# Optimization experiments

Measured on AMD Instinct MI355X. Metric: run time of the kernel, lower is better.

The kernel has to match this reference:

```python
import jax, jax.numpy as jnp
import numpy as np

VOCAB, EMB, UNITS = 50000, 512, 1024
B, T = 2048, 80

def setup_inputs() -> dict:
    key = jax.random.key(0)
    ks = jax.random.split(key, 10)
    s_e = 1.0 / np.sqrt(EMB)
    s_u = 1.0 / np.sqrt(UNITS)
    return {
        "tokens": jax.random.randint(ks[0], (B, T), 0, VOCAB),
        "emb": jax.random.normal(ks[1], (VOCAB, EMB), jnp.float32) * 0.05,
        "W1": jax.random.normal(ks[2], (EMB, UNITS), jnp.float32) * s_e,
        "U1": jax.random.normal(ks[3], (UNITS, UNITS), jnp.float32) * s_u,
        "b1": jnp.zeros((UNITS,), jnp.float32),
        "W2": jax.random.normal(ks[4], (UNITS, UNITS), jnp.float32) * s_u,
        "U2": jax.random.normal(ks[5], (UNITS, UNITS), jnp.float32) * s_u,
        "b2": jnp.zeros((UNITS,), jnp.float32),
        "Wo": jax.random.normal(ks[6], (UNITS, 1), jnp.float32) * s_u,
        "bo": jnp.zeros((1,), jnp.float32),
    }

def _simple_rnn(x_tbd, W, U, b):
    # x_tbd: [T, B, D] time-major input; SimpleRNN: h_t = tanh(x_t W + h_{t-1} U + b)
    B_ = x_tbd.shape[1]
    h0 = jnp.zeros((B_, U.shape[0]), x_tbd.dtype)
    xw = jnp.einsum('tbd,du->tbu', x_tbd, W) + b  # precompute input projection
    def step(h, xw_t):
        h = jnp.tanh(xw_t + h @ U)
        return h, h
    h_last, hs = jax.lax.scan(step, h0, xw)
    return h_last, hs  # hs: [T, B, U]

def reference(tokens, emb, W1, U1, b1, W2, U2, b2, Wo, bo):
    x = emb[tokens]                       # [B, T, E]
    x = jnp.transpose(x, (1, 0, 2))       # [T, B, E] time-major
    _, hs1 = _simple_rnn(x, W1, U1, b1)   # [T, B, U] (return_sequences=True)
    h2, _ = _simple_rnn(hs1, W2, U2, b2)  # [B, U] last state
    logits = h2 @ Wo + bo                 # [B, 1]
    return jax.nn.sigmoid(logits)
```

## Files before the change

kernel.cpp:

```cpp
#include <hip/hip_runtime.h>
#include <math.h>

#define M_TOTAL 2048
#define N_TOTAL 1024
#define TSEQ    80
#define EMB_D   512
#define VOCAB   50000
#define BK      64

typedef __attribute__((ext_vector_type(8))) short bf16x8;
typedef __attribute__((ext_vector_type(4))) float f32x4;

__device__ __forceinline__ ushort f2bf(float f) {
    union { float f; unsigned u; } v; v.f = f;
    unsigned r = v.u + 0x7FFFu + ((v.u >> 16) & 1u);
    return (ushort)(r >> 16);
}
__device__ __forceinline__ float bf2f(ushort h) {
    union { unsigned u; float f; } v; v.u = ((unsigned)h) << 16;
    return v.f;
}
__device__ __forceinline__ void gload_lds16(const ushort* g, ushort* l) {
    __builtin_amdgcn_global_load_lds(
        (const __attribute__((address_space(1))) void*)g,
        (__attribute__((address_space(3))) void*)l, 16, 0, 0);
}
#define VMC6()  asm volatile("s_waitcnt vmcnt(6)" ::: "memory")
#define VMC0()  asm volatile("s_waitcnt vmcnt(0)" ::: "memory")
#define SBAR()  __builtin_amdgcn_s_barrier()
#define SCHED0() __builtin_amdgcn_sched_barrier(0)

__global__ __launch_bounds__(256) void fused_step(
    ushort* __restrict__ xw_h1,
    const ushort* __restrict__ h1prev,
    const ushort* __restrict__ U1T, const float* __restrict__ b1,
    ushort* __restrict__ h2n, const ushort* __restrict__ h2c,
    const ushort* __restrict__ W2T, const ushort* __restrict__ U2T,
    const float* __restrict__ b2, int do_l1, int do_l2)
{
    __shared__ ushort As[3][128 * BK];
    __shared__ ushort Bs[3][64 * BK];
    const int tid = threadIdx.x;
    const int w = tid >> 6, l = tid & 63;
    const int wr = w >> 1, wc = w & 1;
    const int bid = blockIdx.x;
    const int strip = bid & 7;
    const int q = bid >> 3;
    const int layer = q & 1;
    const int rr = q >> 1;
    const int n = strip * 2 + (rr & 1);
    const int m = rr >> 1;
    const int bm0 = m << 7;
    const int bn0 = n << 6;

    if (layer ? !do_l2 : !do_l1) return;

    const int lr = l >> 3;
    const int se = ((l & 7) ^ lr) << 3;

    auto stage = [&](const ushort* __restrict__ A, const ushort* __restrict__ B,
                     int k0, int buf) {
        #pragma unroll
        for (int j = 0; j < 4; ++j) {
            const int rb = w * 32 + j * 8;
            gload_lds16(A + (size_t)(bm0 + rb + lr) * N_TOTAL + k0 + se,
                        &As[buf][rb * BK + l * 8]);
        }
        #pragma unroll
        for (int j = 0; j < 2; ++j) {
            const int rb = w * 16 + j * 8;
            gload_lds16(B + (size_t)(bn0 + rb + lr) * N_TOTAL + k0 + se,
                        &Bs[buf][rb * BK + l * 8]);
        }
    };

    f32x4 acc[4][2] = {};

    auto compute = [&](int buf) {
        #pragma unroll
        for (int kf = 0; kf < 2; ++kf) {
            const int ke = kf * 32 + (l >> 4) * 8;
            bf16x8 a[4], b[2];
            #pragma unroll
            for (int mf = 0; mf < 4; ++mf) {
                const int row = wr * 64 + mf * 16 + (l & 15);
                a[mf] = *(const bf16x8*)&As[buf][row * BK + (ke ^ ((row & 7) << 3))];
            }
            #pragma unroll
            for (int nf = 0; nf < 2; ++nf) {
                const int row = wc * 32 + nf * 16 + (l & 15);
                b[nf] = *(const bf16x8*)&Bs[buf][row * BK + (ke ^ ((row & 7) << 3))];
            }
            #pragma unroll
            for (int mf = 0; mf < 4; ++mf)
                #pragma unroll
                for (int nf = 0; nf < 2; ++nf)
                    acc[mf][nf] = __builtin_amdgcn_mfma_f32_16x16x32_bf16(
                        a[mf], b[nf], acc[mf][nf], 0, 0, 0);
        }
    };

    if (layer == 0) {
        auto stage_cc = [&](int cc, int buf) { stage(h1prev, U1T, cc << 6, buf); };
        stage_cc(0, 0);
        int bufc = 0;
        #pragma unroll
        for (int c = 0; c < 16; ++c) {
            int bufn = bufc + 1; if (bufn == 3) bufn = 0;
            if (c + 1 < 16) { stage_cc(c + 1, bufn); VMC6(); }
            else            { VMC0(); }
            SBAR(); SCHED0();
            compute(bufc);
            bufc = bufn;
        }
        #pragma unroll
        for (int nf = 0; nf < 2; ++nf) {
            const int col = bn0 + wc * 32 + nf * 16 + (l & 15);
            const float bz = b1[col];
            #pragma unroll
            for (int mf = 0; mf < 4; ++mf) {
                const int rb = bm0 + wr * 64 + mf * 16 + (l >> 4) * 4;
                #pragma unroll
                for (int r = 0; r < 4; ++r) {
                    const size_t idx = (size_t)(rb + r) * N_TOTAL + col;
                    xw_h1[idx] = f2bf(tanhf(acc[mf][nf][r] + bf2f(xw_h1[idx]) + bz));
                }
            }
        }
    } else {
        auto stage_cc = [&](int cc, int buf) {
            if (cc < 16) stage(h1prev, W2T, cc << 6, buf);
            else         stage(h2c,    U2T, (cc - 16) << 6, buf);
        };
        stage_cc(0, 0);
        int bufc = 0;
        #pragma unroll
        for (int c = 0; c < 32; ++c) {
            int bufn = bufc + 1; if (bufn == 3) bufn = 0;
            if (c + 1 < 32) { stage_cc(c + 1, bufn); VMC6(); }
            else            { VMC0(); }
            SBAR(); SCHED0();
            compute(bufc);
            bufc = bufn;
        }
        #pragma unroll
        for (int nf = 0; nf < 2; ++nf) {
            const int col = bn0 + wc * 32 + nf * 16 + (l & 15);
            const float bz = b2[col];
            #pragma unroll
            for (int mf = 0; mf < 4; ++mf) {
                const int rb = bm0 + wr * 64 + mf * 16 + (l >> 4) * 4;
                #pragma unroll
                for (int r = 0; r < 4; ++r)
                    h2n[(size_t)(rb + r) * N_TOTAL + col] =
                        f2bf(tanhf(acc[mf][nf][r] + bz));
            }
        }
    }
}

__global__ __launch_bounds__(256) void xw1_gemm(
    ushort* __restrict__ outp,
    const ushort* __restrict__ embb,
    const int* __restrict__ tok,
    const ushort* __restrict__ W1T)
{
    __shared__ ushort As[3][128 * BK];
    __shared__ ushort Bs[3][64 * BK];
    const int tid = threadIdx.x;
    const int w = tid >> 6, l = tid & 63;
    const int wr = w >> 1, wc = w & 1;
    const int bid = blockIdx.x;
    const int strip = bid & 7;
    const int q = bid >> 3;
    const int n = strip * 2 + (q & 1);
    const int m = q >> 1;
    const int bm0 = m << 7;
    const int bn0 = n << 6;

    const int lr = l >> 3;
    const int se = ((l & 7) ^ lr) << 3;

    size_t ga[4];
    #pragma unroll
    for (int j = 0; j < 4; ++j) {
        const int rg = bm0 + w * 32 + j * 8 + lr;
        const int token = tok[(rg & (M_TOTAL - 1)) * TSEQ + (rg >> 11)];
        ga[j] = (size_t)token * EMB_D + se;
    }

    auto stage = [&](int cc, int buf) {
        const int k0 = cc << 6;
        #pragma unroll
        for (int j = 0; j < 4; ++j)
            gload_lds16(embb + ga[j] + k0, &As[buf][(w * 32 + j * 8) * BK + l * 8]);
        #pragma unroll
        for (int j = 0; j < 2; ++j) {
            const int rb = w * 16 + j * 8;
            gload_lds16(W1T + (size_t)(bn0 + rb + lr) * EMB_D + k0 + se,
                        &Bs[buf][rb * BK + l * 8]);
        }
    };

    f32x4 acc[4][2] = {};
    stage(0, 0);
    int bufc = 0;
    #pragma unroll
    for (int c = 0; c < 8; ++c) {
        int bufn = bufc + 1; if (bufn == 3) bufn = 0;
        if (c + 1 < 8) { stage(c + 1, bufn); VMC6(); }
        else           { VMC0(); }
        SBAR(); SCHED0();
        #pragma unroll
        for (int kf = 0; kf < 2; ++kf) {
            const int ke = kf * 32 + (l >> 4) * 8;
            bf16x8 a[4], b[2];
            #pragma unroll
            for (int mf = 0; mf < 4; ++mf) {
                const int row = wr * 64 + mf * 16 + (l & 15);
                a[mf] = *(const bf16x8*)&As[bufc][row * BK + (ke ^ ((row & 7) << 3))];
            }
            #pragma unroll
            for (int nf = 0; nf < 2; ++nf) {
                const int row = wc * 32 + nf * 16 + (l & 15);
                b[nf] = *(const bf16x8*)&Bs[bufc][row * BK + (ke ^ ((row & 7) << 3))];
            }
            #pragma unroll
            for (int mf = 0; mf < 4; ++mf)
                #pragma unroll
                for (int nf = 0; nf < 2; ++nf)
                    acc[mf][nf] = __builtin_amdgcn_mfma_f32_16x16x32_bf16(
                        a[mf], b[nf], acc[mf][nf], 0, 0, 0);
        }
        bufc = bufn;
    }

    #pragma unroll
    for (int nf = 0; nf < 2; ++nf) {
        const int col = bn0 + wc * 32 + nf * 16 + (l & 15);
        #pragma unroll
        for (int mf = 0; mf < 4; ++mf) {
            const int rb = bm0 + wr * 64 + mf * 16 + (l >> 4) * 4;
            #pragma unroll
            for (int r = 0; r < 4; ++r)
                outp[(size_t)(rb + r) * N_TOTAL + col] = f2bf(acc[mf][nf][r]);
        }
    }
}

__global__ __launch_bounds__(256) void emb_convert(
    ushort* __restrict__ dst, const float* __restrict__ src)
{
    const size_t i = ((size_t)blockIdx.x * 256 + threadIdx.x) * 8;
    const float4 v0 = *(const float4*)(src + i);
    const float4 v1 = *(const float4*)(src + i + 4);
    const unsigned w0 = f2bf(v0.x) | (f2bf(v0.y) << 16);
    const unsigned w1 = f2bf(v0.z) | (f2bf(v0.w) << 16);
    const unsigned w2 = f2bf(v1.x) | (f2bf(v1.y) << 16);
    const unsigned w3 = f2bf(v1.z) | (f2bf(v1.w) << 16);
    *(uint4*)(dst + i) = make_uint4(w0, w1, w2, w3);
}

__global__ __launch_bounds__(256) void transpose_convert(
    ushort* __restrict__ outT, const float* __restrict__ in, int K, int N)
{
    __shared__ float tile[64][65];
    const int tiles_n = N >> 6;
    const int k0 = (blockIdx.x / tiles_n) << 6;
    const int n0 = (blockIdx.x % tiles_n) << 6;
    const int tid = threadIdx.x;
    const int r = tid >> 4, c = (tid & 15) << 2;
    #pragma unroll
    for (int i = 0; i < 4; ++i) {
        const float4 v = *(const float4*)(in + (size_t)(k0 + r + i * 16) * N + n0 + c);
        tile[r + i * 16][c + 0] = v.x;
        tile[r + i * 16][c + 1] = v.y;
        tile[r + i * 16][c + 2] = v.z;
        tile[r + i * 16][c + 3] = v.w;
    }
    __syncthreads();
    const int n = tid >> 2, ks = (tid & 3) << 4;
    unsigned pk[8];
    #pragma unroll
    for (int j = 0; j < 8; ++j) {
        const unsigned lo = f2bf(tile[ks + 2 * j][n]);
        const unsigned hi = f2bf(tile[ks + 2 * j + 1][n]);
        pk[j] = lo | (hi << 16);
    }
    ushort* dst = outT + (size_t)(n0 + n) * K + k0 + ks;
    *(uint4*)(dst + 0) = make_uint4(pk[0], pk[1], pk[2], pk[3]);
    *(uint4*)(dst + 8) = make_uint4(pk[4], pk[5], pk[6], pk[7]);
}

__global__ __launch_bounds__(256) void out_kernel(
    float* __restrict__ out, const ushort* __restrict__ h2,
    const float* __restrict__ Wo, const float* __restrict__ bo)
{
    const int row  = blockIdx.x * 4 + (threadIdx.x >> 6);
    const int lane = threadIdx.x & 63;
    const ushort* hr = h2 + (size_t)row * N_TOTAL;
    float s = 0.f;
    for (int k = lane; k < N_TOTAL; k += 64)
        s += bf2f(hr[k]) * Wo[k];
    #pragma unroll
    for (int off = 32; off; off >>= 1)
        s += __shfl_down(s, off);
    if (lane == 0)
        out[row] = 1.f / (1.f + expf(-(s + bo[0])));
}

extern "C" void kernel_launch(void* const* d_in, const int* in_sizes, int n_in,
                              void* d_out, int out_size, void* d_ws, size_t ws_size,
                              hipStream_t stream) {
    const int*   tokens = (const int*)  d_in[0];
    const float* emb    = (const float*)d_in[1];
    const float* W1     = (const float*)d_in[2];
    const float* U1     = (const float*)d_in[3];
    const float* b1     = (const float*)d_in[4];
    const float* W2     = (const float*)d_in[5];
    const float* U2     = (const float*)d_in[6];
    const float* b2     = (const float*)d_in[7];
    const float* Wo     = (const float*)d_in[8];
    const float* bo     = (const float*)d_in[9];
    float* out = (float*)d_out;

    char* ws = (char*)d_ws;
    const size_t HB   = (size_t)M_TOTAL * N_TOTAL * sizeof(ushort);
    const size_t SLAB = (size_t)M_TOTAL * N_TOTAL;
    ushort* h1zero = (ushort*)(ws);
    ushort* h2a    = (ushort*)(ws + 1 * HB);
    ushort* h2b    = (ushort*)(ws + 2 * HB);
    size_t off = 3 * HB;
    ushort* W1T = (ushort*)(ws + off); off += (size_t)N_TOTAL * EMB_D   * 2;
    ushort* U1T = (ushort*)(ws + off); off += (size_t)N_TOTAL * N_TOTAL * 2;
    ushort* W2T = (ushort*)(ws + off); off += (size_t)N_TOTAL * N_TOTAL * 2;
    ushort* U2T = (ushort*)(ws + off); off += (size_t)N_TOTAL * N_TOTAL * 2;
    ushort* embb = (ushort*)(ws + off); off += (size_t)VOCAB * EMB_D * 2;
    ushort* XW1  = (ushort*)(ws + off);

    hipMemsetAsync(h1zero, 0, HB, stream);
    hipMemsetAsync(h2a,    0, HB, stream);

    emb_convert<<<dim3(12500), 256, 0, stream>>>(embb, emb);
    transpose_convert<<<dim3((EMB_D  / 64) * (N_TOTAL / 64)), 256, 0, stream>>>(W1T, W1, EMB_D,   N_TOTAL);
    transpose_convert<<<dim3((N_TOTAL / 64) * (N_TOTAL / 64)), 256, 0, stream>>>(U1T, U1, N_TOTAL, N_TOTAL);
    transpose_convert<<<dim3((N_TOTAL / 64) * (N_TOTAL / 64)), 256, 0, stream>>>(W2T, W2, N_TOTAL, N_TOTAL);
    transpose_convert<<<dim3((N_TOTAL / 64) * (N_TOTAL / 64)), 256, 0, stream>>>(U2T, U2, N_TOTAL, N_TOTAL);

    xw1_gemm<<<dim3((TSEQ * M_TOTAL / 128) * 16), 256, 0, stream>>>(XW1, embb, tokens, W1T);

    ushort* h2c = h2a; ushort* h2n = h2b;
    for (int i = 0; i <= TSEQ; ++i) {
        const int do_l1 = (i < TSEQ) ? 1 : 0;
        const int do_l2 = (i >= 1) ? 1 : 0;
        ushort* slab_i  = (i < TSEQ) ? (XW1 + (size_t)i * SLAB) : XW1;
        const ushort* h1prev = (i == 0) ? h1zero : (XW1 + (size_t)(i - 1) * SLAB);
        fused_step<<<dim3(512), 256, 0, stream>>>(
            slab_i, h1prev, U1T, b1, h2n, h2c, W2T, U2T, b2, do_l1, do_l2);
        if (i >= 1) { ushort* t = h2c; h2c = h2n; h2n = t; }
    }

    out_kernel<<<dim3(M_TOTAL / 4), dim3(256), 0, stream>>>(out, h2c, Wo, bo);
}
```

Measured before the change: 2.428 ms.

## Precompute embedding-projection table, gather per step, and pipeline layer-2 projection separately

Replaces the per-token input projection GEMM (T*B rows) with a GEMM over the vocabulary (emb@W1, about 50k rows) followed by per-step row gathers into a three-slot ring buffer. The layer-2 input projection h1@W2 is split from the recurrent h2@U2 GEMM and skewed across steps with an fp32 intermediate. This lets three independent 128x128-tile GEMM jobs plus a gather run in one launch per step. Tiles grow to 128x128 with a new double/triple-buffered staging schedule. The cost is extra fp32 traffic for the xw2 buffers and a large EW1 table, in exchange for removing the large XW1 GEMM and halving the serial K-depth of the layer-2 work per step.

```diff
diff --git a/kernel.cpp b/kernel.cpp
--- a/kernel.cpp
+++ b/kernel.cpp
@@ -6,6 +6,7 @@
 #define TSEQ    80
 #define EMB_D   512
 #define VOCAB   50000
+#define EW_ROWS 50048
 #define BK      64
 
 typedef __attribute__((ext_vector_type(8))) short bf16x8;
@@ -25,227 +26,196 @@
         (const __attribute__((address_space(1))) void*)g,
         (__attribute__((address_space(3))) void*)l, 16, 0, 0);
 }
-#define VMC6()  asm volatile("s_waitcnt vmcnt(6)" ::: "memory")
+#define VMC4()  asm volatile("s_waitcnt vmcnt(4)" ::: "memory")
 #define VMC0()  asm volatile("s_waitcnt vmcnt(0)" ::: "memory")
 #define SBAR()  __builtin_amdgcn_s_barrier()
 #define SCHED0() __builtin_amdgcn_sched_barrier(0)
 
-__global__ __launch_bounds__(256) void fused_step(
-    ushort* __restrict__ xw_h1,
-    const ushort* __restrict__ h1prev,
-    const ushort* __restrict__ U1T, const float* __restrict__ b1,
-    ushort* __restrict__ h2n, const ushort* __restrict__ h2c,
-    const ushort* __restrict__ W2T, const ushort* __restrict__ U2T,
-    const float* __restrict__ b2, int do_l1, int do_l2)
-{
-    __shared__ ushort As[3][128 * BK];
-    __shared__ ushort Bs[3][64 * BK];
-    const int tid = threadIdx.x;
-    const int w = tid >> 6, l = tid & 63;
+template<int NC>
+__device__ __forceinline__ void gemm_core(
+    f32x4 (&acc)[4][4],
+    const ushort* __restrict__ A, const size_t* __restrict__ ga,
+    const ushort* __restrict__ B, const size_t* __restrict__ gb,
+    int w, int l,
+    ushort (*As)[128 * BK], ushort (*Bs)[128 * BK])
+{
     const int wr = w >> 1, wc = w & 1;
-    const int bid = blockIdx.x;
-    const int strip = bid & 7;
-    const int q = bid >> 3;
-    const int layer = q & 1;
-    const int rr = q >> 1;
-    const int n = strip * 2 + (rr & 1);
-    const int m = rr >> 1;
-    const int bm0 = m << 7;
-    const int bn0 = n << 6;
-
-    if (layer ? !do_l2 : !do_l1) return;
-
-    const int lr = l >> 3;
-    const int se = ((l & 7) ^ lr) << 3;
-
-    auto stage = [&](const ushort* __restrict__ A, const ushort* __restrict__ B,
-                     int k0, int buf) {
-        #pragma unroll
-        for (int j = 0; j < 4; ++j) {
-            const int rb = w * 32 + j * 8;
-            gload_lds16(A + (size_t)(bm0 + rb + lr) * N_TOTAL + k0 + se,
-                        &As[buf][rb * BK + l * 8]);
-        }
-        #pragma unroll
-        for (int j = 0; j < 2; ++j) {
-            const int rb = w * 16 + j * 8;
-            gload_lds16(B + (size_t)(bn0 + rb + lr) * N_TOTAL + k0 + se,
-                        &Bs[buf][rb * BK + l * 8]);
-        }
+    auto stA = [&](int c, int buf) {
+        const int k0 = c << 6;
+        #pragma unroll
+        for (int j = 0; j < 4; ++j)
+            gload_lds16(A + ga[j] + k0, &As[buf][(w * 32 + j * 8) * BK + l * 8]);
     };
-
-    f32x4 acc[4][2] = {};
-
-    auto compute = [&](int buf) {
+    auto stB = [&](int c, int buf) {
+        const int k0 = c << 6;
+        #pragma unroll
+        for (int j = 0; j < 4; ++j)
+            gload_lds16(B + gb[j] + k0, &Bs[buf][(w * 32 + j * 8) * BK + l * 8]);
+    };
+    stA(0, 0); stB(0, 0); stA(1, 1);
+    #pragma unroll
+    for (int c = 0; c < NC; ++c) {
+        if (c + 1 < NC) { VMC4(); } else { VMC0(); }
+        SBAR(); SCHED0();
+        if (c + 1 < NC) stB(c + 1, (c + 1) & 1);
+        if (c + 2 < NC) stA(c + 2, (c + 2) % 3);
         #pragma unroll
         for (int kf = 0; kf < 2; ++kf) {
             const int ke = kf * 32 + (l >> 4) * 8;
-            bf16x8 a[4], b[2];
+            bf16x8 a[4], b[4];
             #pragma unroll
             for (int mf = 0; mf < 4; ++mf) {
                 const int row = wr * 64 + mf * 16 + (l & 15);
-                a[mf] = *(const bf16x8*)&As[buf][row * BK + (ke ^ ((row & 7) << 3))];
+                a[mf] = *(const bf16x8*)&As[c % 3][row * BK + (ke ^ ((row & 7) << 3))];
             }
             #pragma unroll
-            for (int nf = 0; nf < 2; ++nf) {
-                const int row = wc * 32 + nf * 16 + (l & 15);
-                b[nf] = *(const bf16x8*)&Bs[buf][row * BK + (ke ^ ((row & 7) << 3))];
+            for (int nf = 0; nf < 4; ++nf) {
+                const int row = wc * 64 + nf * 16 + (l & 15);
+                b[nf] = *(const bf16x8*)&Bs[c & 1][row * BK + (ke ^ ((row & 7) << 3))];
             }
             #pragma unroll
             for (int mf = 0; mf < 4; ++mf)
                 #pragma unroll
-                for (int nf = 0; nf < 2; ++nf)
+                for (int nf = 0; nf < 4; ++nf)
                     acc[mf][nf] = __builtin_amdgcn_mfma_f32_16x16x32_bf16(
                         a[mf], b[nf], acc[mf][nf], 0, 0, 0);
         }
-    };
-
-    if (layer == 0) {
-        auto stage_cc = [&](int cc, int buf) { stage(h1prev, U1T, cc << 6, buf); };
-        stage_cc(0, 0);
-        int bufc = 0;
-        #pragma unroll
-        for (int c = 0; c < 16; ++c) {
-            int bufn = bufc + 1; if (bufn == 3) bufn = 0;
-            if (c + 1 < 16) { stage_cc(c + 1, bufn); VMC6(); }
-            else            { VMC0(); }
-            SBAR(); SCHED0();
-            compute(bufc);
-            bufc = bufn;
-        }
-        #pragma unroll
-        for (int nf = 0; nf < 2; ++nf) {
-            const int col = bn0 + wc * 32 + nf * 16 + (l & 15);
-            const float bz = b1[col];
-            #pragma unroll
-            for (int mf = 0; mf < 4; ++mf) {
-                const int rb = bm0 + wr * 64 + mf * 16 + (l >> 4) * 4;
-                #pragma unroll
-                for (int r = 0; r < 4; ++r) {
-                    const size_t idx = (size_t)(rb + r) * N_TOTAL + col;
-                    xw_h1[idx] = f2bf(tanhf(acc[mf][nf][r] + bf2f(xw_h1[idx]) + bz));
-                }
+    }
+}
+
+__global__ __launch_bounds__(256) void fused_step(
+    const ushort* __restrict__ EW1,
+    const int* __restrict__ tok,
+    const ushort* __restrict__ sl_prev,
+    ushort* __restrict__ sl_cur,
+    ushort* __restrict__ sl_next,
+    const ushort* __restrict__ U1T, const float* __restrict__ b1,
+    const ushort* __restrict__ W2T,
+    float* __restrict__ xw2_dst,
+    const float* __restrict__ xw2_src,
+    const ushort* __restrict__ U2T, const float* __restrict__ b2,
+    const ushort* __restrict__ h2prev,
+    ushort* __restrict__ h2dst,
+    int i)
+{
+    __shared__ ushort As[3][128 * BK];
+    __shared__ ushort Bs[2][128 * BK];
+    const int tid = threadIdx.x;
+    const int bid = blockIdx.x;
+
+    if (bid >= 384) {
+        if (i > TSEQ - 2) return;
+        const int b = (bid - 384) * 32 + (tid >> 3);
+        const int token = tok[b * TSEQ + i + 1];
+        const uint4* src = (const uint4*)(EW1 + (size_t)token * N_TOTAL);
+        uint4* dst = (uint4*)(sl_next + (size_t)b * N_TOTAL);
+        #pragma unroll
+        for (int g = 0; g < 16; ++g)
+            dst[(tid & 7) + g * 8] = src[(tid & 7) + g * 8];
+        return;
+    }
+
+    const int w = tid >> 6, l = tid & 63;
+    const int n = bid & 7, rest = bid >> 3;
+    const int job = rest % 3;
+    const int m = rest / 3;
+    const int bm0 = m << 7, bn0 = n << 7;
+
+    if (job == 0 && i > TSEQ - 1) return;
+    if (job == 1 && (i < 1 || i > TSEQ)) return;
+    if (job == 2 && i < 2) return;
+
+    const ushort* A; const ushort* B;
+    if (job == 0)      { A = sl_prev; B = U1T; }
+    else if (job == 1) { A = sl_prev; B = W2T; }
+    else               { A = h2prev;  B = U2T; }
+
+    const int lr = l >> 3;
+    const int se = ((l & 7) ^ lr) << 3;
+    size_t ga[4], gb[4];
+    #pragma unroll
+    for (int j = 0; j < 4; ++j) {
+        ga[j] = (size_t)(bm0 + w * 32 + j * 8 + lr) * N_TOTAL + se;
+        gb[j] = (size_t)(bn0 + w * 32 + j * 8 + lr) * N_TOTAL + se;
+    }
+
+    f32x4 acc[4][4] = {};
+    gemm_core<16>(acc, A, ga, B, gb, w, l, As, Bs);
+
+    const int wr = w >> 1, wc = w & 1;
+    #pragma unroll
+    for (int nf = 0; nf < 4; ++nf) {
+        const int col = bn0 + wc * 64 + nf * 16 + (l & 15);
+        #pragma unroll
+        for (int mf = 0; mf < 4; ++mf) {
+            const int rb = bm0 + wr * 64 + mf * 16 + (l >> 4) * 4;
+            #pragma unroll
+            for (int r = 0; r < 4; ++r) {
+                const size_t idx = (size_t)(rb + r) * N_TOTAL + col;
+                if (job == 0)
+                    sl_cur[idx] = f2bf(tanhf(acc[mf][nf][r] + bf2f(sl_cur[idx]) + b1[col]));
+                else if (job == 1)
+                    xw2_dst[idx] = acc[mf][nf][r];
+                else
+                    h2dst[idx] = f2bf(tanhf(acc[mf][nf][r] + xw2_src[idx] + b2[col]));
             }
         }
-    } else {
-        auto stage_cc = [&](int cc, int buf) {
-            if (cc < 16) stage(h1prev, W2T, cc << 6, buf);
-            else         stage(h2c,    U2T, (cc - 16) << 6, buf);
-        };
-        stage_cc(0, 0);
-        int bufc = 0;
-        #pragma unroll
-        for (int c = 0; c < 32; ++c) {
-            int bufn = bufc + 1; if (bufn == 3) bufn = 0;
-            if (c + 1 < 32) { stage_cc(c + 1, bufn); VMC6(); }
-            else            { VMC0(); }
-            SBAR(); SCHED0();
-            compute(bufc);
-            bufc = bufn;
-        }
-        #pragma unroll
-        for (int nf = 0; nf < 2; ++nf) {
-            const int col = bn0 + wc * 32 + nf * 16 + (l & 15);
-            const float bz = b2[col];
-            #pragma unroll
-            for (int mf = 0; mf < 4; ++mf) {
-                const int rb = bm0 + wr * 64 + mf * 16 + (l >> 4) * 4;
-                #pragma unroll
-                for (int r = 0; r < 4; ++r)
-                    h2n[(size_t)(rb + r) * N_TOTAL + col] =
-                        f2bf(tanhf(acc[mf][nf][r] + bz));
-            }
-        }
-    }
-}
-
-__global__ __launch_bounds__(256) void xw1_gemm(
-    ushort* __restrict__ outp,
+    }
+}
+
+__global__ __launch_bounds__(256) void ew1_gemm(
+    ushort* __restrict__ EW1,
     const ushort* __restrict__ embb,
-    const int* __restrict__ tok,
     const ushort* __restrict__ W1T)
 {
     __shared__ ushort As[3][128 * BK];
-    __shared__ ushort Bs[3][64 * BK];
+    __shared__ ushort Bs[2][128 * BK];
     const int tid = threadIdx.x;
     const int w = tid >> 6, l = tid & 63;
-    const int wr = w >> 1, wc = w & 1;
     const int bid = blockIdx.x;
-    const int strip = bid & 7;
-    const int q = bid >> 3;
-    const int n = strip * 2 + (q & 1);
-    const int m = q >> 1;
-    const int bm0 = m << 7;
-    const int bn0 = n << 6;
+    const int n = bid & 7, m = bid >> 3;
+    const int bm0 = m << 7, bn0 = n << 7;
 
     const int lr = l >> 3;
     const int se = ((l & 7) ^ lr) << 3;
-
-    size_t ga[4];
+    size_t ga[4], gb[4];
     #pragma unroll
     for (int j = 0; j < 4; ++j) {
-        const int rg = bm0 + w * 32 + j * 8 + lr;
-        const int token = tok[(rg & (M_TOTAL - 1)) * TSEQ + (rg >> 11)];
-        ga[j] = (size_t)token * EMB_D + se;
-    }
-
-    auto stage = [&](int cc, int buf) {
-        const int k0 = cc << 6;
-        #pragma unroll
-        for (int j = 0; j < 4; ++j)
-            gload_lds16(embb + ga[j] + k0, &As[buf][(w * 32 + j * 8) * BK + l * 8]);
-        #pragma unroll
-        for (int j = 0; j < 2; ++j) {
-            const int rb = w * 16 + j * 8;
-            gload_lds16(W1T + (size_t)(bn0 + rb + lr) * EMB_D + k0 + se,
-                        &Bs[buf][rb * BK + l * 8]);
-        }
-    };
-
-    f32x4 acc[4][2] = {};
-    stage(0, 0);
-    int bufc = 0;
-    #pragma unroll
-    for (int c = 0; c < 8; ++c) {
-        int bufn = bufc + 1; if (bufn == 3) bufn = 0;
-        if (c + 1 < 8) { stage(c + 1, bufn); VMC6(); }
-        else           { VMC0(); }
-        SBAR(); SCHED0();
-        #pragma unroll
-        for (int kf = 0; kf < 2; ++kf) {
-            const int ke = kf * 32 + (l >> 4) * 8;
-            bf16x8 a[4], b[2];
-            #pragma unroll
-            for (int mf = 0; mf < 4; ++mf) {
-                const int row = wr * 64 + mf * 16 + (l & 15);
-                a[mf] = *(const bf16x8*)&As[bufc][row * BK + (ke ^ ((row & 7) << 3))];
-            }
-            #pragma unroll
-            for (int nf = 0; nf < 2; ++nf) {
-                const int row = wc * 32 + nf * 16 + (l & 15);
-                b[nf] = *(const bf16x8*)&Bs[bufc][row * BK + (ke ^ ((row & 7) << 3))];
-            }
-            #pragma unroll
-            for (int mf = 0; mf < 4; ++mf)
-                #pragma unroll
-                for (int nf = 0; nf < 2; ++nf)
-                    acc[mf][nf] = __builtin_amdgcn_mfma_f32_16x16x32_bf16(
-                        a[mf], b[nf], acc[mf][nf], 0, 0, 0);
-        }
-        bufc = bufn;
-    }
-
-    #pragma unroll
-    for (int nf = 0; nf < 2; ++nf) {
-        const int col = bn0 + wc * 32 + nf * 16 + (l & 15);
+        int row = bm0 + w * 32 + j * 8 + lr;
+        if (row >= VOCAB) row = VOCAB - 1;
+        ga[j] = (size_t)row * EMB_D + se;
+        gb[j] = (size_t)(bn0 + w * 32 + j * 8 + lr) * EMB_D + se;
+    }
+
+    f32x4 acc[4][4] = {};
+    gemm_core<8>(acc, embb, ga, W1T, gb, w, l, As, Bs);
+
+    const int wr = w >> 1, wc = w & 1;
+    #pragma unroll
+    for (int nf = 0; nf < 4; ++nf) {
+        const int col = bn0 + wc * 64 + nf * 16 + (l & 15);
         #pragma unroll
         for (int mf = 0; mf < 4; ++mf) {
             const int rb = bm0 + wr * 64 + mf * 16 + (l >> 4) * 4;
             #pragma unroll
             for (int r = 0; r < 4; ++r)
-                outp[(size_t)(rb + r) * N_TOTAL + col] = f2bf(acc[mf][nf][r]);
+                if (rb + r < VOCAB)
+                    EW1[(size_t)(rb + r) * N_TOTAL + col] = f2bf(acc[mf][nf][r]);
         }
     }
+}
+
+__global__ __launch_bounds__(256) void gather_xw1(
+    ushort* __restrict__ dst, const ushort* __restrict__ EW1,
+    const int* __restrict__ tok, int t)
+{
+    const int b = blockIdx.x * 32 + (threadIdx.x >> 3);
+    const int token = tok[b * TSEQ + t];
+    const uint4* src = (const uint4*)(EW1 + (size_t)token * N_TOTAL);
+    uint4* d = (uint4*)(dst + (size_t)b * N_TOTAL);
+    #pragma unroll
+    for (int g = 0; g < 16; ++g)
+        d[(threadIdx.x & 7) + g * 8] = src[(threadIdx.x & 7) + g * 8];
 }
 
 __global__ __launch_bounds__(256) void emb_convert(
@@ -325,21 +295,29 @@
     float* out = (float*)d_out;
 
     char* ws = (char*)d_ws;
-    const size_t HB   = (size_t)M_TOTAL * N_TOTAL * sizeof(ushort);
-    const size_t SLAB = (size_t)M_TOTAL * N_TOTAL;
-    ushort* h1zero = (ushort*)(ws);
-    ushort* h2a    = (ushort*)(ws + 1 * HB);
-    ushort* h2b    = (ushort*)(ws + 2 * HB);
-    size_t off = 3 * HB;
+    const size_t HB = (size_t)M_TOTAL * N_TOTAL * sizeof(ushort);
+    size_t off = 0;
+    ushort* h1zero = (ushort*)(ws + off); off += HB;
+    ushort* h2x0   = (ushort*)(ws + off); off += HB;
+    ushort* h2x1   = (ushort*)(ws + off); off += HB;
+    ushort* ring0  = (ushort*)(ws + off); off += HB;
+    ushort* ring1  = (ushort*)(ws + off); off += HB;
+    ushort* ring2  = (ushort*)(ws + off); off += HB;
+    float*  xw2f0  = (float*)(ws + off);  off += (size_t)M_TOTAL * N_TOTAL * 4;
+    float*  xw2f1  = (float*)(ws + off);  off += (size_t)M_TOTAL * N_TOTAL * 4;
     ushort* W1T = (ushort*)(ws + off); off += (size_t)N_TOTAL * EMB_D   * 2;
     ushort* U1T = (ushort*)(ws + off); off += (size_t)N_TOTAL * N_TOTAL * 2;
     ushort* W2T = (ushort*)(ws + off); off += (size_t)N_TOTAL * N_TOTAL * 2;
     ushort* U2T = (ushort*)(ws + off); off += (size_t)N_TOTAL * N_TOTAL * 2;
     ushort* embb = (ushort*)(ws + off); off += (size_t)VOCAB * EMB_D * 2;
-    ushort* XW1  = (ushort*)(ws + off);
+    ushort* EW1  = (ushort*)(ws + off); off += (size_t)EW_ROWS * N_TOTAL * 2;
+
+    ushort* ring[3] = { ring0, ring1, ring2 };
+    float*  xw2f[2] = { xw2f0, xw2f1 };
+    ushort* h2x[2]  = { h2x0, h2x1 };
 
     hipMemsetAsync(h1zero, 0, HB, stream);
-    hipMemsetAsync(h2a,    0, HB, stream);
+    hipMemsetAsync(h2x1,   0, HB, stream);
 
     emb_convert<<<dim3(12500), 256, 0, stream>>>(embb, emb);
     transpose_convert<<<dim3((EMB_D  / 64) * (N_TOTAL / 64)), 256, 0, stream>>>(W1T, W1, EMB_D,   N_TOTAL);
@@ -347,18 +325,21 @@
     transpose_convert<<<dim3((N_TOTAL / 64) * (N_TOTAL / 64)), 256, 0, stream>>>(W2T, W2, N_TOTAL, N_TOTAL);
     transpose_convert<<<dim3((N_TOTAL / 64) * (N_TOTAL / 64)), 256, 0, stream>>>(U2T, U2, N_TOTAL, N_TOTAL);
 
-    xw1_gemm<<<dim3((TSEQ * M_TOTAL / 128) * 16), 256, 0, stream>>>(XW1, embb, tokens, W1T);
-
-    ushort* h2c = h2a; ushort* h2n = h2b;
-    for (int i = 0; i <= TSEQ; ++i) {
-        const int do_l1 = (i < TSEQ) ? 1 : 0;
-        const int do_l2 = (i >= 1) ? 1 : 0;
-        ushort* slab_i  = (i < TSEQ) ? (XW1 + (size_t)i * SLAB) : XW1;
-        const ushort* h1prev = (i == 0) ? h1zero : (XW1 + (size_t)(i - 1) * SLAB);
-        fused_step<<<dim3(512), 256, 0, stream>>>(
-            slab_i, h1prev, U1T, b1, h2n, h2c, W2T, U2T, b2, do_l1, do_l2);
-        if (i >= 1) { ushort* t = h2c; h2c = h2n; h2n = t; }
-    }
-
-    out_kernel<<<dim3(M_TOTAL / 4), dim3(256), 0, stream>>>(out, h2c, Wo, bo);
-}
+    ew1_gemm<<<dim3((EW_ROWS / 128) * 8), 256, 0, stream>>>(EW1, embb, W1T);
+    gather_xw1<<<dim3(64), 256, 0, stream>>>(ring[0], EW1, tokens, 0);
+
+    for (int i = 0; i <= TSEQ + 1; ++i) {
+        const ushort* sl_prev = (i == 0) ? h1zero : ring[(i - 1) % 3];
+        ushort* sl_cur  = ring[i % 3];
+        ushort* sl_next = ring[(i + 1) % 3];
+        float* xw2_dst  = xw2f[(i - 1) & 1];
+        const float* xw2_src = xw2f[(i - 2) & 1];
+        const ushort* h2prev = h2x[(i - 3) & 1];
+        ushort* h2dst = h2x[(i - 2) & 1];
+        fused_step<<<dim3(448), 256, 0, stream>>>(
+            EW1, tokens, sl_prev, sl_cur, sl_next,
+            U1T, b1, W2T, xw2_dst, xw2_src, U2T, b2, h2prev, h2dst, i);
+    }
+
+    out_kernel<<<dim3(M_TOTAL / 4), dim3(256), 0, stream>>>(out, h2x[1], Wo, bo);
+}
```

After: 3.529 ms. +45.3%, slower.
